# Kernel tuning notes

Measured on AMD Instinct MI355X. Metric: run time of the kernel, lower is better.

## Reference

```python
import jax, jax.numpy as jnp
import numpy as np

NUM_HEADS = 4

def setup_inputs() -> dict:
    key = jax.random.key(0)
    ks = jax.random.split(key, 5)
    B, N, C = 2, 4096, 256
    s = 0.02
    return {
        "x": jax.random.normal(ks[0], (B, N, C), dtype=jnp.float32),
        "qkv_w": jax.random.normal(ks[1], (3 * C, C), dtype=jnp.float32) * s,
        "qkv_b": jax.random.normal(ks[2], (3 * C,), dtype=jnp.float32) * s,
        "out_w": jax.random.normal(ks[3], (C, C), dtype=jnp.float32) * s,
        "out_b": jax.random.normal(ks[4], (C,), dtype=jnp.float32) * s,
    }

def reference(x, qkv_w, qkv_b, out_w, out_b):
    # x: [B, N, C]; manual multi-head self-attention (eval mode, dropout off)
    B, N, C = x.shape
    H = NUM_HEADS
    D = C // H
    qkv = x @ qkv_w.T + qkv_b                      # [B, N, 3C]
    qkv = qkv.reshape(B, N, 3, H, D)
    qkv = jnp.transpose(qkv, (2, 0, 3, 1, 4))      # [3, B, H, N, D]
    q, k, v = qkv[0], qkv[1], qkv[2]
    scale = D ** -0.5
    attn = jnp.einsum('bhnd,bhmd->bhnm', q, k) * scale  # [B, H, N, N]
    attn = jax.nn.softmax(attn, axis=-1)
    out = jnp.einsum('bhnm,bhmd->bhnd', attn, v)   # [B, H, N, D]
    out = jnp.transpose(out, (0, 2, 1, 3)).reshape(B, N, C)
    return out @ out_w.T + out_b
```

## Files before the change

kernel.cpp:

```cpp
#include <hip/hip_runtime.h>

typedef __bf16 bf16x8 __attribute__((ext_vector_type(8)));
typedef float f32x4 __attribute__((ext_vector_type(4)));

#define MFMA_BF16(a, b, c) __builtin_amdgcn_mfma_f32_16x16x32_bf16((a), (b), (c), 0, 0, 0)

#define C1 0.18033688f

static __device__ __forceinline__ unsigned short f2bf(float f) {
    unsigned int u = __float_as_uint(f);
    unsigned int r = (u + 0x7fffu + ((u >> 16) & 1u)) >> 16;
    return (unsigned short)r;
}
static __device__ __forceinline__ float bf2f(unsigned short us) {
    return __uint_as_float(((unsigned int)us) << 16);
}
static __device__ __forceinline__ float exp2_hw(float x) {
    float r;
    asm("v_exp_f32 %0, %1" : "=v"(r) : "v"(x));
    return r;
}
static __device__ __forceinline__ unsigned pack_rh(float a, float b) {
    return __byte_perm(__float_as_uint(a) + 0x8000u, __float_as_uint(b) + 0x8000u, 0x7632);
}
static __device__ __forceinline__ void gload16(const void* g, void* l) {
    __builtin_amdgcn_global_load_lds(
        (const __attribute__((address_space(1))) unsigned int*)g,
        (__attribute__((address_space(3))) unsigned int*)l, 16, 0, 0);
}

static __device__ __forceinline__ void conv_seg8(const void* src, unsigned short* dst, int n,
                                                 int lb, bool f32) {
    const int base = lb * 2048 + (int)threadIdx.x * 8;
    if (base < n) {
        if (f32) {
            const float4 u0 = *(const float4*)((const float*)src + base);
            const float4 u1 = *(const float4*)((const float*)src + base + 4);
            uint4 p;
            p.x = pack_rh(u0.x, u0.y);
            p.y = pack_rh(u0.z, u0.w);
            p.z = pack_rh(u1.x, u1.y);
            p.w = pack_rh(u1.z, u1.w);
            *(uint4*)(dst + base) = p;
        } else {
            *(uint4*)(dst + base) = *(const uint4*)((const unsigned short*)src + base);
        }
    }
}

__global__ __launch_bounds__(256) void convert_kernel(
    const void* __restrict__ x, const void* __restrict__ qw, const void* __restrict__ qb,
    const void* __restrict__ ow, const void* __restrict__ ob,
    unsigned short* __restrict__ xb, unsigned short* __restrict__ qwb,
    unsigned short* __restrict__ qbb, unsigned short* __restrict__ owb,
    unsigned short* __restrict__ obb, int* __restrict__ flag) {
    __shared__ int tot;
    if (threadIdx.x == 0) tot = 0;
    __syncthreads();
    {
        unsigned short v = ((const unsigned short*)x)[threadIdx.x];
        int e = (v >> 7) & 0xFF;
        if (e >= 195) atomicAdd(&tot, 1);
    }
    __syncthreads();
    const bool f32 = (tot >= 8);
    if (blockIdx.x == 0 && threadIdx.x == 0) flag[0] = f32 ? 1 : 0;

    const int bid = blockIdx.x;
    if (bid < 1024)       conv_seg8(x,  xb,  2097152, bid,        f32);
    else if (bid < 1120)  conv_seg8(qw, qwb, 196608,  bid - 1024, f32);
    else if (bid < 1121)  conv_seg8(qb, qbb, 768,     bid - 1120, f32);
    else if (bid < 1153)  conv_seg8(ow, owb, 65536,   bid - 1121, f32);
    else                  conv_seg8(ob, obb, 256,     bid - 1153, f32);
}

template <bool QKV>
__global__ __launch_bounds__(256) void gemm_kernel(
    const unsigned short* __restrict__ A, const unsigned short* __restrict__ W,
    const unsigned short* __restrict__ bias, unsigned short* __restrict__ Cb,
    float* __restrict__ Cf, const int* __restrict__ flag,
    unsigned short* __restrict__ Vt, int Nout) {
    constexpr int K = 256;
    __shared__ __align__(16) char sm[16384];

    const int tid = threadIdx.x;
    const int lane = tid & 63;
    const int wv = tid >> 6;
    const int m16 = lane & 15;
    const int quad = lane >> 4;
    const int bm = blockIdx.x * 64;
    const int bn = blockIdx.y * 64;

    int bgo[2], blo[2];
#pragma unroll
    for (int i = 0; i < 2; i++) {
        const int c = wv * 128 + i * 64 + lane;
        const int r = c >> 3, g = (c & 7) ^ (r & 7);
        bgo[i] = r * (K * 2) + g * 16;
        blo[i] = c * 16;
    }
    int bro[4][2];
#pragma unroll
    for (int t = 0; t < 4; t++)
#pragma unroll
        for (int ks = 0; ks < 2; ks++) {
            const int row = t * 16 + m16;
            bro[t][ks] = row * 64 + ((4 * ks + quad) ^ (m16 & 7)) * 8;
        }

    const char* bg = (const char*)(W + (size_t)bn * K);
    const unsigned short* ap = A + (size_t)(bm + wv * 16 + m16) * K + quad * 8;

#pragma unroll
    for (int i = 0; i < 2; i++) gload16(bg + bgo[i], sm + blo[i]);
    bf16x8 a0 = *(const bf16x8*)(ap);
    bf16x8 a1 = *(const bf16x8*)(ap + 32);

    f32x4 acc[4] = {};
#pragma unroll
    for (int kb = 0; kb < 4; kb++) {
        __syncthreads();
        const int cur = kb & 1;
        bf16x8 a0n, a1n;
        if (kb < 3) {
            bg += 128;
            char* Bdst = sm + (cur ^ 1) * 8192;
#pragma unroll
            for (int i = 0; i < 2; i++) gload16(bg + bgo[i], Bdst + blo[i]);
            a0n = *(const bf16x8*)(ap + (kb + 1) * 64);
            a1n = *(const bf16x8*)(ap + (kb + 1) * 64 + 32);
        }
        const unsigned short* Blds = (const unsigned short*)(sm + cur * 8192);
#pragma unroll
        for (int ks = 0; ks < 2; ks++) {
            const bf16x8 a = ks ? a1 : a0;
#pragma unroll
            for (int t = 0; t < 4; t++) {
                const bf16x8 b = *(const bf16x8*)(Blds + bro[t][ks]);
                acc[t] = MFMA_BF16(a, b, acc[t]);
            }
        }
        if (kb < 3) {
            a0 = a0n;
            a1 = a1n;
        }
    }

    if (QKV && bn >= 512) {
        __syncthreads();
        unsigned short* tr = (unsigned short*)sm;
        const int lr = wv * 16 + quad * 4;
#pragma unroll
        for (int t = 0; t < 4; t++) {
            const float bv = bf2f(bias[bn + t * 16 + m16]);
            uint2 w;
            w.x = pack_rh(acc[t][0] + bv, acc[t][1] + bv);
            w.y = pack_rh(acc[t][2] + bv, acc[t][3] + bv);
            *(uint2*)&tr[(t * 16 + m16) * 72 + lr] = w;
        }
        __syncthreads();
        const int d = tid >> 2;
        const int ch = (tid & 3) * 16;
        const uint4 o4a = *(const uint4*)&tr[d * 72 + ch];
        const uint4 o4b = *(const uint4*)&tr[d * 72 + ch + 8];
        const int hh = (bn - 512) >> 6;
        const int bb = bm >> 12, n0 = bm & 4095;
        const int nn = n0 + ch;
        const int kt = nn >> 7, koff = nn & 127;
        unsigned short* vdst =
            &Vt[(size_t)(((bb * 4 + hh) * 32 + kt) * 64 + d) * 128 + koff];
        *(uint4*)(vdst) = o4a;
        *(uint4*)(vdst + 8) = o4b;
        return;
    }

    const bool outf = (!QKV) && (flag != nullptr) && (*flag != 0);
    const int row0 = bm + wv * 16 + quad * 4;
#pragma unroll
    for (int t = 0; t < 4; t++) {
        const int col = bn + t * 16 + m16;
        const float bv = bf2f(bias[col]);
        float v[4];
#pragma unroll
        for (int r = 0; r < 4; r++) v[r] = acc[t][r] + bv;
        if (QKV) {
            const float sc = (col < 256) ? C1 : 1.0f;
#pragma unroll
            for (int r = 0; r < 4; r++)
                Cb[(size_t)(row0 + r) * 768 + col] = f2bf(v[r] * sc);
        } else {
            if (outf) {
#pragma unroll
                for (int r = 0; r < 4; r++) Cf[(size_t)(row0 + r) * Nout + col] = v[r];
            } else {
#pragma unroll
                for (int r = 0; r < 4; r++) Cb[(size_t)(row0 + r) * Nout + col] = f2bf(v[r]);
            }
        }
    }
}

#define ZERO_S(S)                                                     \
    do {                                                              \
        _Pragma("unroll") for (int mb = 0; mb < 2; mb++)              \
            _Pragma("unroll") for (int j = 0; j < 4; j++)             \
                S[mb][j] = (f32x4){0.f, 0.f, 0.f, 0.f};               \
    } while (0)

#define LDK(KP)                                                                \
    do {                                                                       \
        kf[0][0] = *(const bf16x8*)((KP));                                     \
        kf[0][1] = *(const bf16x8*)((KP) + 64);                                \
        kf[1][0] = *(const bf16x8*)((KP) + 24576);                             \
        kf[1][1] = *(const bf16x8*)((KP) + 24576 + 64);                        \
    } while (0)

#define QKT(S)                                                                 \
    do {                                                                       \
        __builtin_amdgcn_s_setprio(1);                                         \
        _Pragma("unroll") for (int mb = 0; mb < 2; mb++)                       \
            _Pragma("unroll") for (int ks = 0; ks < 2; ks++) {                 \
                _Pragma("unroll") for (int j = 0; j < 4; j++)                  \
                    S[mb][j] = MFMA_BF16(kf[mb][ks], qf[j][ks], S[mb][j]);     \
            }                                                                  \
        __builtin_amdgcn_s_setprio(0);                                         \
    } while (0)

#define EXPP(S, PA)                                                            \
    do {                                                                       \
        _Pragma("unroll") for (int j = 0; j < 4; j++) {                        \
            const float e0 = exp2_hw(S[0][j][0]);                              \
            const float e1 = exp2_hw(S[0][j][1]);                              \
            const float e2 = exp2_hw(S[0][j][2]);                              \
            const float e3 = exp2_hw(S[0][j][3]);                              \
            const float e4 = exp2_hw(S[1][j][0]);                              \
            const float e5 = exp2_hw(S[1][j][1]);                              \
            const float e6 = exp2_hw(S[1][j][2]);                              \
            const float e7 = exp2_hw(S[1][j][3]);                              \
            uint4 pw_;                                                         \
            pw_.x = pack_rh(e0, e1);                                           \
            pw_.y = pack_rh(e2, e3);                                           \
            pw_.z = pack_rh(e4, e5);                                           \
            pw_.w = pack_rh(e6, e7);                                           \
            PA[j] = *(const bf16x8*)&pw_;                                      \
        }                                                                      \
    } while (0)

#define PVACC(PA, VBASE)                                                       \
    do {                                                                       \
        const unsigned short* Vb_ = (const unsigned short*)(VBASE);            \
        __builtin_amdgcn_s_setprio(1);                                         \
        _Pragma("unroll") for (int j = 0; j < 4; j++)                          \
            o1[j] = MFMA_BF16(PA[j], ones, o1[j]);                             \
        _Pragma("unroll") for (int t = 0; t < 4; t++) {                        \
            const uint2 va_ = *(const uint2*)(Vb_ + vroA[t]);                  \
            const uint2 vc_ = *(const uint2*)(Vb_ + (vroA[t] ^ 16));           \
            uint4 vv_;                                                         \
            vv_.x = va_.x;                                                     \
            vv_.y = va_.y;                                                     \
            vv_.z = vc_.x;                                                     \
            vv_.w = vc_.y;                                                     \
            const bf16x8 vb_ = *(const bf16x8*)&vv_;                           \
            _Pragma("unroll") for (int j = 0; j < 4; j++)                      \
                o[j][t] = MFMA_BF16(PA[j], vb_, o[j][t]);                      \
        }                                                                      \
        __builtin_amdgcn_s_setprio(0);                                         \
    } while (0)

#define GLV(DST)                                                               \
    {                                                                          \
        _Pragma("unroll") for (int i = 0; i < 4; i++)                          \
            gload16(vgn + vgo[i], (DST) + vlo[i]);                             \
        vgn += 16384;                                                          \
    }

__global__ __launch_bounds__(256, 2) void attn_kernel(
    const unsigned short* __restrict__ qkv, const unsigned short* __restrict__ Vt,
    unsigned short* __restrict__ attn, int iters) {
    const int N = 4096, C3 = 768;
    __shared__ __align__(16) char sm[32768];

    const int tid = threadIdx.x;
    const int lane = tid & 63;
    const int wv = tid >> 6;
    const int m16 = lane & 15;
    const int quad = lane >> 4;

    const int bh = blockIdx.x & 7;
    const int qt = blockIdx.x >> 3;
    const int b = bh >> 2, h = bh & 3;

    bf16x8 qf[4][2];
#pragma unroll
    for (int j = 0; j < 4; j++)
#pragma unroll
        for (int ks = 0; ks < 2; ks++)
            qf[j][ks] = *(const bf16x8*)(qkv + ((size_t)b * N + qt * 64 + j * 16 + m16) * C3 +
                                         h * 64 + ks * 32 + quad * 8);

    uint4 ones_u;
    ones_u.x = ones_u.y = ones_u.z = ones_u.w = 0x3F803F80u;
    const bf16x8 ones = *(const bf16x8*)&ones_u;

    int vgo[4], vlo[4];
#pragma unroll
    for (int i = 0; i < 4; i++) {
        const int c = i * 64 + lane;
        const int d = c >> 2, js = c & 3, jg = js ^ ((d >> 2) & 3);
        vgo[i] = d * 256 + wv * 64 + jg * 16;
        vlo[i] = c * 16;
    }
    int vroA[4];
#pragma unroll
    for (int t = 0; t < 4; t++) {
        const int d = t * 16 + m16;
        const int c0 = (quad >> 1) ^ ((d >> 2) & 3);
        vroA[t] = d * 32 + c0 * 8 + (quad & 1) * 4;
    }

    char* Vreg0 = sm + wv * 8192;

    const char* kbn = (const char*)(qkv + (size_t)b * N * C3 + 256 + h * 64) +
                      (size_t)(wv * 32 + m16) * 1536 + quad * 16;
    const char* vgn = (const char*)(Vt + (size_t)bh * 262144);

    f32x4 o[4][4] = {};
    f32x4 o1[4] = {};
    f32x4 sA[2][4], sB[2][4];
    bf16x8 pa[4];
    bf16x8 kf[2][2];

    LDK(kbn);
    GLV(Vreg0);
    GLV(Vreg0 + 4096);
    ZERO_S(sA);
    QKT(sA);
    LDK(kbn + 196608);
    kbn += 2 * 196608;

    for (int t2 = 0; t2 < 15; ++t2) {
        asm volatile("s_waitcnt vmcnt(0)" ::: "memory");
        ZERO_S(sB);
        QKT(sB);
        EXPP(sA, pa);
        PVACC(pa, Vreg0);
        asm volatile("s_waitcnt lgkmcnt(0)" ::: "memory");
        GLV(Vreg0);
        LDK(kbn);
        kbn += 196608;

        asm volatile("s_waitcnt vmcnt(0)" ::: "memory");
        ZERO_S(sA);
        QKT(sA);
        EXPP(sB, pa);
        PVACC(pa, Vreg0 + 4096);
        asm volatile("s_waitcnt lgkmcnt(0)" ::: "memory");
        GLV(Vreg0 + 4096);
        LDK(kbn);
        kbn += 196608;
    }
    asm volatile("s_waitcnt vmcnt(0)" ::: "memory");
    ZERO_S(sB);
    QKT(sB);
    EXPP(sA, pa);
    PVACC(pa, Vreg0);
    EXPP(sB, pa);
    PVACC(pa, Vreg0 + 4096);

    __syncthreads();
    float* Ored = (float*)sm;
    float* lsum = (float*)(sm + 16384);
    if (m16 == 0) {
#pragma unroll
        for (int j = 0; j < 4; j++)
#pragma unroll
            for (int r = 0; r < 4; r++)
                lsum[wv * 64 + j * 16 + quad * 4 + r] = o1[j][r];
    }
    const int row = tid >> 4;
    const int col = (tid & 15) * 4;
#pragma unroll
    for (int j = 0; j < 4; j++) {
#pragma unroll
        for (int t = 0; t < 4; t++)
#pragma unroll
            for (int r = 0; r < 4; r++)
                Ored[(wv * 16 + quad * 4 + r) * 64 + t * 16 + m16] = o[j][t][r];
        __syncthreads();
        f32x4 sum = *(f32x4*)&Ored[row * 64 + col];
        sum += *(f32x4*)&Ored[1024 + row * 64 + col];
        sum += *(f32x4*)&Ored[2048 + row * 64 + col];
        sum += *(f32x4*)&Ored[3072 + row * 64 + col];
        const float lq = lsum[j * 16 + row] + lsum[64 + j * 16 + row] +
                         lsum[128 + j * 16 + row] + lsum[192 + j * 16 + row];
        const int n = qt * 64 + j * 16 + row;
        const float inv = 1.0f / lq;
        uint2 w;
        w.x = pack_rh(sum[0] * inv, sum[1] * inv);
        w.y = pack_rh(sum[2] * inv, sum[3] * inv);
        *(uint2*)&attn[((size_t)b * N + n) * 256 + h * 64 + col] = w;
        __syncthreads();
    }
}

extern "C" void kernel_launch(void* const* d_in, const int* in_sizes, int n_in,
                              void* d_out, int out_size, void* d_ws, size_t ws_size,
                              hipStream_t stream) {
    const int B = 2, N = 4096, H = 4;
    const int M = B * N;

    char* wsb = (char*)d_ws;
    int* flag = (int*)wsb;
    unsigned short* xb      = (unsigned short*)(wsb + 64);
    unsigned short* qwb     = xb + 2097152;
    unsigned short* qbb     = qwb + 196608;
    unsigned short* owb     = qbb + 768;
    unsigned short* obb     = owb + 65536;
    unsigned short* qkv_ws  = obb + 256;
    unsigned short* Vt_ws   = qkv_ws + 6291456;
    unsigned short* attn_ws = Vt_ws + 2097152;

    convert_kernel<<<1154, 256, 0, stream>>>(d_in[0], d_in[1], d_in[2], d_in[3], d_in[4],
                                             xb, qwb, qbb, owb, obb, flag);

    gemm_kernel<true><<<dim3(M / 64, 768 / 64), 256, 0, stream>>>(
        xb, qwb, qbb, qkv_ws, nullptr, nullptr, Vt_ws, 768);

    attn_kernel<<<512, 256, 0, stream>>>(qkv_ws, Vt_ws, attn_ws, 32);

    gemm_kernel<false><<<dim3(M / 64, 256 / 64), 256, 0, stream>>>(
        attn_ws, owb, obb, (unsigned short*)d_out, (float*)d_out, flag, nullptr, 256);
}
```

Measured before the change: 136.3 us.

## Double-buffer K fragments and use partial vmcnt waits in attention loop

Splits the K register fragments into two buffers so the next tile's K load is issued right after the current QK^T and can overlap with the exp and PV work. The full vmcnt(0) waits become counted partial waits (vmcnt 8/12), so only the V tile being consumed has to have landed. The goal is to hide global-load latency for K and V within each wave. The cost is more VGPRs for the second K buffer, which may pressure occupancy under launch_bounds(256,2), and correctness now depends on the exact vmcnt counts.

Measured after the change: 136.1 us. About the same (-0.2%).

```diff
diff --git a/kernel.cpp b/kernel.cpp
--- a/kernel.cpp
+++ b/kernel.cpp
@@ -207,21 +207,21 @@
                 S[mb][j] = (f32x4){0.f, 0.f, 0.f, 0.f};               \
     } while (0)
 
-#define LDK(KP)                                                                \
+#define LDK(KF, KP)                                                            \
     do {                                                                       \
-        kf[0][0] = *(const bf16x8*)((KP));                                     \
-        kf[0][1] = *(const bf16x8*)((KP) + 64);                                \
-        kf[1][0] = *(const bf16x8*)((KP) + 24576);                             \
-        kf[1][1] = *(const bf16x8*)((KP) + 24576 + 64);                        \
+        KF[0][0] = *(const bf16x8*)((KP));                                     \
+        KF[0][1] = *(const bf16x8*)((KP) + 64);                                \
+        KF[1][0] = *(const bf16x8*)((KP) + 24576);                             \
+        KF[1][1] = *(const bf16x8*)((KP) + 24576 + 64);                        \
     } while (0)
 
-#define QKT(S)                                                                 \
+#define QKT(S, KF)                                                             \
     do {                                                                       \
         __builtin_amdgcn_s_setprio(1);                                         \
         _Pragma("unroll") for (int mb = 0; mb < 2; mb++)                       \
             _Pragma("unroll") for (int ks = 0; ks < 2; ks++) {                 \
                 _Pragma("unroll") for (int j = 0; j < 4; j++)                  \
-                    S[mb][j] = MFMA_BF16(kf[mb][ks], qf[j][ks], S[mb][j]);     \
+                    S[mb][j] = MFMA_BF16(KF[mb][ks], qf[j][ks], S[mb][j]);     \
             }                                                                  \
         __builtin_amdgcn_s_setprio(0);                                         \
     } while (0)
@@ -274,6 +274,9 @@
         vgn += 16384;                                                          \
     }
 
+#define WAITV(N) asm volatile("s_waitcnt vmcnt(" #N ")" ::: "memory")
+#define WAITL    asm volatile("s_waitcnt lgkmcnt(0)" ::: "memory")
+
 __global__ __launch_bounds__(256, 2) void attn_kernel(
     const unsigned short* __restrict__ qkv, const unsigned short* __restrict__ Vt,
     unsigned short* __restrict__ attn, int iters) {
@@ -328,43 +331,61 @@
     f32x4 o1[4] = {};
     f32x4 sA[2][4], sB[2][4];
     bf16x8 pa[4];
-    bf16x8 kf[2][2];
-
-    LDK(kbn);
+    bf16x8 kfa[2][2], kfb[2][2];
+
+    LDK(kfa, kbn);  kbn += 196608;
+    LDK(kfb, kbn);  kbn += 196608;
     GLV(Vreg0);
     GLV(Vreg0 + 4096);
     ZERO_S(sA);
-    QKT(sA);
-    LDK(kbn + 196608);
-    kbn += 2 * 196608;
-
-    for (int t2 = 0; t2 < 15; ++t2) {
-        asm volatile("s_waitcnt vmcnt(0)" ::: "memory");
+    QKT(sA, kfa);
+
+    ZERO_S(sB);
+    QKT(sB, kfb);
+    LDK(kfa, kbn);  kbn += 196608;
+    EXPP(sA, pa);
+    WAITV(8);
+    PVACC(pa, Vreg0);
+    WAITL;
+    GLV(Vreg0);
+
+    for (int p = 0; p < 14; ++p) {
+        ZERO_S(sA);
+        QKT(sA, kfa);
+        LDK(kfb, kbn);  kbn += 196608;
+        EXPP(sB, pa);
+        WAITV(12);
+        PVACC(pa, Vreg0 + 4096);
+        WAITL;
+        GLV(Vreg0 + 4096);
+
         ZERO_S(sB);
-        QKT(sB);
+        QKT(sB, kfb);
+        LDK(kfa, kbn);  kbn += 196608;
         EXPP(sA, pa);
+        WAITV(12);
         PVACC(pa, Vreg0);
-        asm volatile("s_waitcnt lgkmcnt(0)" ::: "memory");
+        WAITL;
         GLV(Vreg0);
-        LDK(kbn);
-        kbn += 196608;
-
-        asm volatile("s_waitcnt vmcnt(0)" ::: "memory");
-        ZERO_S(sA);
-        QKT(sA);
-        EXPP(sB, pa);
-        PVACC(pa, Vreg0 + 4096);
-        asm volatile("s_waitcnt lgkmcnt(0)" ::: "memory");
-        GLV(Vreg0 + 4096);
-        LDK(kbn);
-        kbn += 196608;
-    }
-    asm volatile("s_waitcnt vmcnt(0)" ::: "memory");
+    }
+
+    ZERO_S(sA);
+    QKT(sA, kfa);
+    LDK(kfb, kbn);
+    EXPP(sB, pa);
+    WAITV(12);
+    PVACC(pa, Vreg0 + 4096);
+    WAITL;
+    GLV(Vreg0 + 4096);
+
     ZERO_S(sB);
-    QKT(sB);
+    QKT(sB, kfb);
     EXPP(sA, pa);
+    WAITV(8);
     PVACC(pa, Vreg0);
+
     EXPP(sB, pa);
+    WAITV(0);
     PVACC(pa, Vreg0 + 4096);
 
     __syncthreads();
```
